# Optimization experiments

Measured on AMD Instinct MI355X. Metric: run time of the kernel, lower is better.

## Reference

```python
import jax, jax.numpy as jnp
import numpy as np

N_NODES = 100000
N_EDGES = 1600000
HIDDEN = 512
LOWER = 128
NUM_RELS = 6


def setup_inputs() -> dict:
    key = jax.random.key(0)
    ks = jax.random.split(key, 16)
    glorot = lambda k, shape: jax.random.normal(k, shape, jnp.float32) * (2.0 / (shape[-2] + shape[-1])) ** 0.5
    return {
        "h_origin": jax.random.normal(ks[0], (N_NODES, HIDDEN), jnp.float32),
        "edge_src": jax.random.randint(ks[1], (N_EDGES,), 0, N_NODES, jnp.int32),
        "edge_dst": jax.random.randint(ks[2], (N_EDGES,), 0, N_NODES, jnp.int32),
        "edge_type": jax.random.randint(ks[3], (N_EDGES,), 0, NUM_RELS, jnp.int32),
        "W_lower": glorot(ks[4], (HIDDEN, LOWER)),
        "b_lower": jnp.zeros((LOWER,), jnp.float32),
        "W1": glorot(ks[5], (NUM_RELS, LOWER, LOWER)),
        "b1": jnp.zeros((LOWER,), jnp.float32),
        "W2": glorot(ks[6], (NUM_RELS, LOWER, LOWER)),
        "b2": jnp.zeros((LOWER,), jnp.float32),
        "W3": glorot(ks[7], (NUM_RELS, LOWER, LOWER)),
        "b3": jnp.zeros((LOWER,), jnp.float32),
        "W_upper": glorot(ks[8], (LOWER, HIDDEN)),
        "b_upper": jnp.zeros((HIDDEN,), jnp.float32),
        "W_skip": glorot(ks[9], (HIDDEN, HIDDEN)),
        "b_skip": jnp.zeros((HIDDEN,), jnp.float32),
    }


def _ngcn_layer(h, W, b, edge_src, edge_dst, edge_type, n_nodes):
    # R-GCN layer: msg_e = h[src_e] @ W[rel_e]; h'_v = relu(sum_{e->v} msg_e + b)
    # Equivalent grouped form: transform all nodes by all relations (dense GEMMs),
    # then gather per-edge by (rel, src) -- same math as per-edge bmm.
    t = jnp.einsum("nd,rde->rne", h, W)          # [R, N, out]
    msg = t[edge_type, edge_src]                   # [E, out] gather
    agg = jax.ops.segment_sum(msg, edge_dst, num_segments=n_nodes)  # [N, out]
    return jax.nn.relu(agg + b)


def reference(h_origin, edge_src, edge_dst, edge_type,
              W_lower, b_lower, W1, b1, W2, b2, W3, b3,
              W_upper, b_upper, W_skip, b_skip):
    n_nodes = h_origin.shape[0]
    # lower: Linear + ReLU (hidden -> lower)
    h = jax.nn.relu(h_origin @ W_lower + b_lower)
    # three NGCN (R-GCN) layers, num_rels = 6
    h = _ngcn_layer(h, W1, b1, edge_src, edge_dst, edge_type, n_nodes)
    h = _ngcn_layer(h, W2, b2, edge_src, edge_dst, edge_type, n_nodes)
    h = _ngcn_layer(h, W3, b3, edge_src, edge_dst, edge_type, n_nodes)
    # upper(h) + skipper(origin): bg.ndata['h'] = upper(h) + skipper(origin_ndata)
    out = jax.nn.relu(h @ W_upper + b_upper) + jax.nn.relu(h_origin @ W_skip + b_skip)
    return out
```

## Files before the change

### kernel.cpp

```cpp
#include <hip/hip_runtime.h>
#include <hip/hip_bf16.h>

#define NN 100000
#define NE 1600000
#define HID 512
#define LOW 128
#define NR  6
#define NBINS (NN * NR)

typedef short  bf16x8 __attribute__((ext_vector_type(8)));
typedef float  f32x4  __attribute__((ext_vector_type(4)));
typedef float  f32x8  __attribute__((ext_vector_type(8)));
typedef unsigned short u16x8 __attribute__((ext_vector_type(8)));

__device__ __forceinline__ unsigned short f2bf(float x) {
    __hip_bfloat16 h = __float2bfloat16(x);
    return __builtin_bit_cast(unsigned short, h);
}
__device__ __forceinline__ float bf2f(unsigned short u) {
    return __builtin_bit_cast(float, (unsigned int)u << 16);
}
__device__ __forceinline__ f32x8 cvt8(u16x8 u) {
    f32x8 r;
    #pragma unroll
    for (int i = 0; i < 8; ++i) r[i] = bf2f(u[i]);
    return r;
}

template<int ITERS>
__device__ __forceinline__ void stage_rows(const unsigned short* __restrict__ G,
                                           int r0, int k0, int Kstride, int Rmax,
                                           char* lds_base, int tid)
{
    #pragma unroll
    for (int is = 0; is < ITERS; ++is) {
        int L   = is * 4096 + tid * 16;
        int row = L >> 7;
        int c   = ((L >> 4) & 7) ^ (row & 7);
        int gr  = r0 + row;
        gr = (gr < Rmax) ? gr : (Rmax - 1);
        const char* src = (const char*)G + ((size_t)gr * Kstride + k0) * 2 + c * 16;
        __builtin_amdgcn_global_load_lds(
            (const __attribute__((address_space(1))) void*)src,
            (__attribute__((address_space(3))) void*)(lds_base + is * 4096 + (tid & 192) * 16),
            16, 0, 0);
    }
}

__device__ __forceinline__ bf16x8 lds_frag(const char* lds_base, int row, int clog)
{
    return *(const bf16x8*)(lds_base + row * 128 + ((clog ^ (row & 7)) << 4));
}

__global__ __launch_bounds__(256, 2)
void gemm_bf16(const unsigned short* __restrict__ A,
               const unsigned short* __restrict__ Bt,
               const float* __restrict__ bias,
               unsigned short* __restrict__ C,
               int M, int N, int K)
{
    __shared__ __align__(16) char lA[16384];
    __shared__ __align__(16) char lB[16384];

    const int tid  = threadIdx.x;
    const int lane = tid & 63;
    const int wid  = tid >> 6;
    const int wm   = wid >> 1;
    const int wn   = wid & 1;
    const int m0   = blockIdx.y * 128;
    const int n0   = blockIdx.x * 128;

    f32x4 acc[4][4] = {};

    for (int k0 = 0; k0 < K; k0 += 64) {
        stage_rows<4>(A,  m0, k0, K, M, lA, tid);
        stage_rows<4>(Bt, n0, k0, K, N, lB, tid);
        __syncthreads();
        #pragma unroll
        for (int kk = 0; kk < 2; ++kk) {
            const int clog = kk * 4 + (lane >> 4);
            bf16x8 af[4], bfr[4];
            #pragma unroll
            for (int i = 0; i < 4; ++i)
                af[i] = lds_frag(lA, wm * 64 + i * 16 + (lane & 15), clog);
            #pragma unroll
            for (int j = 0; j < 4; ++j)
                bfr[j] = lds_frag(lB, wn * 64 + j * 16 + (lane & 15), clog);
            #pragma unroll
            for (int i = 0; i < 4; ++i)
                #pragma unroll
                for (int j = 0; j < 4; ++j)
                    acc[i][j] = __builtin_amdgcn_mfma_f32_16x16x32_bf16(
                        af[i], bfr[j], acc[i][j], 0, 0, 0);
        }
        __syncthreads();
    }

    const int col_l = lane & 15;
    const int rgrp  = lane >> 4;
    #pragma unroll
    for (int i = 0; i < 4; ++i) {
        #pragma unroll
        for (int j = 0; j < 4; ++j) {
            int col  = n0 + wn * 64 + j * 16 + col_l;
            float bv = bias[col];
            #pragma unroll
            for (int r = 0; r < 4; ++r) {
                int row = m0 + wm * 64 + i * 16 + rgrp * 4 + r;
                if (row < M)
                    C[(size_t)row * N + col] = f2bf(fmaxf(acc[i][j][r] + bv, 0.f));
            }
        }
    }
}

__global__ __launch_bounds__(256, 2)
void gemm_out_fused(const unsigned short* __restrict__ h,
                    const unsigned short* __restrict__ Wut,
                    const float* __restrict__ bu,
                    const unsigned short* __restrict__ hob,
                    const unsigned short* __restrict__ Wst,
                    const float* __restrict__ bs,
                    float* __restrict__ out, int M)
{
    __shared__ __align__(16) char lA[16384];
    __shared__ __align__(16) char lB[16384];

    const int tid  = threadIdx.x;
    const int lane = tid & 63;
    const int wid  = tid >> 6;
    const int wm   = wid >> 1;
    const int wn   = wid & 1;

    const int nwg  = gridDim.x;
    const int cpx  = nwg >> 3;
    const int idx  = (blockIdx.x & 7) * cpx + (blockIdx.x >> 3);
    const int m0   = (idx >> 2) * 128;
    const int n0   = (idx & 3) * 128;

    f32x4 acc1[4][4] = {};
    f32x4 acc2[4][4] = {};

    for (int k0 = 0; k0 < LOW; k0 += 64) {
        stage_rows<4>(h,   m0, k0, LOW, M,   lA, tid);
        stage_rows<4>(Wut, n0, k0, LOW, HID, lB, tid);
        __syncthreads();
        #pragma unroll
        for (int kk = 0; kk < 2; ++kk) {
            const int clog = kk * 4 + (lane >> 4);
            bf16x8 af[4], bfr[4];
            #pragma unroll
            for (int i = 0; i < 4; ++i)
                af[i] = lds_frag(lA, wm * 64 + i * 16 + (lane & 15), clog);
            #pragma unroll
            for (int j = 0; j < 4; ++j)
                bfr[j] = lds_frag(lB, wn * 64 + j * 16 + (lane & 15), clog);
            #pragma unroll
            for (int i = 0; i < 4; ++i)
                #pragma unroll
                for (int j = 0; j < 4; ++j)
                    acc1[i][j] = __builtin_amdgcn_mfma_f32_16x16x32_bf16(
                        af[i], bfr[j], acc1[i][j], 0, 0, 0);
        }
        __syncthreads();
    }
    for (int k0 = 0; k0 < HID; k0 += 64) {
        stage_rows<4>(hob, m0, k0, HID, M,   lA, tid);
        stage_rows<4>(Wst, n0, k0, HID, HID, lB, tid);
        __syncthreads();
        #pragma unroll
        for (int kk = 0; kk < 2; ++kk) {
            const int clog = kk * 4 + (lane >> 4);
            bf16x8 af[4], bfr[4];
            #pragma unroll
            for (int i = 0; i < 4; ++i)
                af[i] = lds_frag(lA, wm * 64 + i * 16 + (lane & 15), clog);
            #pragma unroll
            for (int j = 0; j < 4; ++j)
                bfr[j] = lds_frag(lB, wn * 64 + j * 16 + (lane & 15), clog);
            #pragma unroll
            for (int i = 0; i < 4; ++i)
                #pragma unroll
                for (int j = 0; j < 4; ++j)
                    acc2[i][j] = __builtin_amdgcn_mfma_f32_16x16x32_bf16(
                        af[i], bfr[j], acc2[i][j], 0, 0, 0);
        }
        __syncthreads();
    }

    const int col_l = lane & 15;
    const int rgrp  = lane >> 4;
    #pragma unroll
    for (int i = 0; i < 4; ++i) {
        #pragma unroll
        for (int j = 0; j < 4; ++j) {
            int col   = n0 + wn * 64 + j * 16 + col_l;
            float bv1 = bu[col], bv2 = bs[col];
            #pragma unroll
            for (int r = 0; r < 4; ++r) {
                int row = m0 + wm * 64 + i * 16 + rgrp * 4 + r;
                if (row < M) {
                    float v = fmaxf(acc1[i][j][r] + bv1, 0.f) +
                              fmaxf(acc2[i][j][r] + bv2, 0.f);
                    __builtin_nontemporal_store(v, &out[(size_t)row * HID + col]);
                }
            }
        }
    }
}

__global__ __launch_bounds__(256)
void conv_f32_bf16(const float4* __restrict__ in, ushort4* __restrict__ out, int n4)
{
    for (int i = blockIdx.x * 256 + threadIdx.x; i < n4; i += gridDim.x * 256) {
        float4 v = in[i];
        ushort4 o;
        o.x = f2bf(v.x); o.y = f2bf(v.y); o.z = f2bf(v.z); o.w = f2bf(v.w);
        out[i] = o;
    }
}

__global__ __launch_bounds__(256)
void transpose_bf16(const float* __restrict__ W, unsigned short* __restrict__ Wt,
                    int R, int C)
{
    int idx = blockIdx.x * 256 + threadIdx.x;
    if (idx < R * C) {
        int r = idx / C, c = idx - r * C;
        Wt[(size_t)c * R + r] = f2bf(W[idx]);
    }
}

#define SCAN_VT 8
#define SCAN_BS 256
#define SCAN_CHUNK (SCAN_VT * SCAN_BS)
#define SCAN_NB ((NBINS + SCAN_CHUNK - 1) / SCAN_CHUNK)

__global__ __launch_bounds__(256)
void k_hist(const int* __restrict__ dst, const int* __restrict__ typ,
            int* __restrict__ deg, int E)
{
    int e = blockIdx.x * 256 + threadIdx.x;
    if (e < E) atomicAdd(&deg[dst[e] * NR + typ[e]], 1);
}

__global__ __launch_bounds__(SCAN_BS)
void k_scan_part(const int* __restrict__ deg, int* __restrict__ blocksum, int n)
{
    __shared__ int ps[SCAN_BS];
    const int t = threadIdx.x;
    const int lo = blockIdx.x * SCAN_CHUNK + t * SCAN_VT;
    int s = 0;
    #pragma unroll
    for (int k = 0; k < SCAN_VT; ++k) {
        int i = lo + k;
        if (i < n) s += deg[i];
    }
    ps[t] = s;
    __syncthreads();
    for (int off = SCAN_BS / 2; off > 0; off >>= 1) {
        if (t < off) ps[t] += ps[t + off];
        __syncthreads();
    }
    if (t == 0) blocksum[blockIdx.x] = ps[0];
}

__global__ __launch_bounds__(64)
void k_scan_mid(const int* __restrict__ blocksum, int* __restrict__ blockoff,
                int* __restrict__ rowstart, int nb, int n)
{
    if (threadIdx.x == 0) {
        int run = 0;
        for (int i = 0; i < nb; ++i) { blockoff[i] = run; run += blocksum[i]; }
        rowstart[n] = run;
    }
}

__global__ __launch_bounds__(SCAN_BS)
void k_scan_final(const int* __restrict__ deg, const int* __restrict__ blockoff,
                  int* __restrict__ rowstart, int* __restrict__ cursor, int n)
{
    __shared__ int ps[SCAN_BS];
    const int t = threadIdx.x;
    const int lo = blockIdx.x * SCAN_CHUNK + t * SCAN_VT;
    int local[SCAN_VT];
    int s = 0;
    #pragma unroll
    for (int k = 0; k < SCAN_VT; ++k) {
        int i = lo + k;
        int v = (i < n) ? deg[i] : 0;
        local[k] = v;
        s += v;
    }
    ps[t] = s;
    __syncthreads();
    for (int off = 1; off < SCAN_BS; off <<= 1) {
        int v = (t >= off) ? ps[t - off] : 0;
        __syncthreads();
        ps[t] += v;
        __syncthreads();
    }
    int run = blockoff[blockIdx.x] + ((t > 0) ? ps[t - 1] : 0);
    #pragma unroll
    for (int k = 0; k < SCAN_VT; ++k) {
        int i = lo + k;
        if (i < n) {
            rowstart[i] = run;
            cursor[i]   = run;
            run += local[k];
        }
    }
}

__global__ __launch_bounds__(256)
void k_fill(const int* __restrict__ src, const int* __restrict__ dst,
            const int* __restrict__ typ, int* __restrict__ cursor,
            int* __restrict__ list, int E)
{
    int e = blockIdx.x * 256 + threadIdx.x;
    if (e < E) {
        int pos = atomicAdd(&cursor[dst[e] * NR + typ[e]], 1);
        list[pos] = src[e];
    }
}

__global__ __launch_bounds__(256)
void gather_agg(const unsigned short* __restrict__ h,
                const int* __restrict__ rowstart,
                const int* __restrict__ list,
                unsigned short* __restrict__ S)
{
    const int v = (blockIdx.x * 256 + threadIdx.x) >> 4;
    const int lane = threadIdx.x & 15;
    const u16x8* hp = (const u16x8*)h;

    const int b0 = rowstart[v * NR + 0];
    const int b1 = rowstart[v * NR + 1];
    const int b2 = rowstart[v * NR + 2];
    const int b3 = rowstart[v * NR + 3];
    const int b4 = rowstart[v * NR + 4];
    const int b5 = rowstart[v * NR + 5];
    const int b6 = rowstart[v * NR + 6];
    const int n0 = b1 - b0, n1 = b2 - b1, n2 = b3 - b2;
    const int n3 = b4 - b3, n4 = b5 - b4, n5 = b6 - b5;
    const int kmax = max(max(max(n0, n1), max(n2, n3)), max(n4, n5));

    f32x8 a0 = {}, a1 = {}, a2 = {}, a3 = {}, a4 = {}, a5 = {};

    for (int k = 0; k < kmax; ++k) {
        int i0 = (k < n0) ? (b0 + k) : 0;
        int i1 = (k < n1) ? (b1 + k) : 0;
        int i2 = (k < n2) ? (b2 + k) : 0;
        int i3 = (k < n3) ? (b3 + k) : 0;
        int i4 = (k < n4) ? (b4 + k) : 0;
        int i5 = (k < n5) ? (b5 + k) : 0;
        int s0 = list[i0], s1 = list[i1], s2 = list[i2];
        int s3 = list[i3], s4 = list[i4], s5 = list[i5];
        u16x8 u0 = hp[(size_t)s0 * 16 + lane];
        u16x8 u1 = hp[(size_t)s1 * 16 + lane];
        u16x8 u2 = hp[(size_t)s2 * 16 + lane];
        u16x8 u3 = hp[(size_t)s3 * 16 + lane];
        u16x8 u4 = hp[(size_t)s4 * 16 + lane];
        u16x8 u5 = hp[(size_t)s5 * 16 + lane];
        if (k < n0) a0 += cvt8(u0);
        if (k < n1) a1 += cvt8(u1);
        if (k < n2) a2 += cvt8(u2);
        if (k < n3) a3 += cvt8(u3);
        if (k < n4) a4 += cvt8(u4);
        if (k < n5) a5 += cvt8(u5);
    }

    u16x8* o = (u16x8*)(S + (size_t)v * (NR * LOW));
    u16x8 w;
    #pragma unroll
    for (int i = 0; i < 8; ++i) w[i] = f2bf(a0[i]);
    __builtin_nontemporal_store(w, &o[0 * 16 + lane]);
    #pragma unroll
    for (int i = 0; i < 8; ++i) w[i] = f2bf(a1[i]);
    __builtin_nontemporal_store(w, &o[1 * 16 + lane]);
    #pragma unroll
    for (int i = 0; i < 8; ++i) w[i] = f2bf(a2[i]);
    __builtin_nontemporal_store(w, &o[2 * 16 + lane]);
    #pragma unroll
    for (int i = 0; i < 8; ++i) w[i] = f2bf(a3[i]);
    __builtin_nontemporal_store(w, &o[3 * 16 + lane]);
    #pragma unroll
    for (int i = 0; i < 8; ++i) w[i] = f2bf(a4[i]);
    __builtin_nontemporal_store(w, &o[4 * 16 + lane]);
    #pragma unroll
    for (int i = 0; i < 8; ++i) w[i] = f2bf(a5[i]);
    __builtin_nontemporal_store(w, &o[5 * 16 + lane]);
}

extern "C" void kernel_launch(void* const* d_in, const int* in_sizes, int n_in,
                              void* d_out, int out_size, void* d_ws, size_t ws_size,
                              hipStream_t stream)
{
    (void)in_sizes; (void)n_in; (void)out_size; (void)ws_size;

    const float* h_origin = (const float*)d_in[0];
    const int*   esrc     = (const int*)d_in[1];
    const int*   edst     = (const int*)d_in[2];
    const int*   etyp     = (const int*)d_in[3];
    const float* W_lower  = (const float*)d_in[4];
    const float* b_lower  = (const float*)d_in[5];
    const float* Wl[3]    = {(const float*)d_in[6], (const float*)d_in[8], (const float*)d_in[10]};
    const float* bl[3]    = {(const float*)d_in[7], (const float*)d_in[9], (const float*)d_in[11]};
    const float* W_upper  = (const float*)d_in[12];
    const float* b_upper  = (const float*)d_in[13];
    const float* W_skip   = (const float*)d_in[14];
    const float* b_skip   = (const float*)d_in[15];
    float*       out      = (float*)d_out;

    unsigned short* hob = (unsigned short*)d_ws;
    unsigned short* h   = hob + (size_t)NN * HID;
    unsigned short* S   = h + (size_t)NN * LOW;
    unsigned short* wlt = S + (size_t)NN * NR * LOW;
    unsigned short* w1t = wlt + (size_t)LOW * HID;
    unsigned short* w2t = w1t + (size_t)LOW * NR * LOW;
    unsigned short* w3t = w2t + (size_t)LOW * NR * LOW;
    unsigned short* wut = w3t + (size_t)LOW * NR * LOW;
    unsigned short* wst = wut + (size_t)HID * LOW;
    int* deg      = (int*)(wst + (size_t)HID * HID);
    int* rowstart = deg + NBINS;
    int* cursor   = rowstart + NBINS + 1;
    int* list     = cursor + NBINS;
    int* blocksum = list + NE;
    int* blockoff = blocksum + SCAN_NB;
    unsigned short* wtL[3] = {w1t, w2t, w3t};

    const unsigned eBlocks = (unsigned)((NE + 255) / 256);
    const unsigned mBlocks = (unsigned)((NN + 127) / 128);

    conv_f32_bf16<<<dim3(2048), dim3(256), 0, stream>>>(
        (const float4*)h_origin, (ushort4*)hob, NN * HID / 4);
    transpose_bf16<<<dim3((HID * LOW + 255) / 256), dim3(256), 0, stream>>>(
        W_lower, wlt, HID, LOW);
    for (int L = 0; L < 3; ++L)
        transpose_bf16<<<dim3((NR * LOW * LOW + 255) / 256), dim3(256), 0, stream>>>(
            Wl[L], wtL[L], NR * LOW, LOW);
    transpose_bf16<<<dim3((LOW * HID + 255) / 256), dim3(256), 0, stream>>>(
        W_upper, wut, LOW, HID);
    transpose_bf16<<<dim3((HID * HID + 255) / 256), dim3(256), 0, stream>>>(
        W_skip, wst, HID, HID);

    hipMemsetAsync(deg, 0, NBINS * sizeof(int), stream);
    k_hist<<<dim3(eBlocks), dim3(256), 0, stream>>>(edst, etyp, deg, NE);
    k_scan_part<<<dim3(SCAN_NB), dim3(SCAN_BS), 0, stream>>>(deg, blocksum, NBINS);
    k_scan_mid<<<dim3(1), dim3(64), 0, stream>>>(blocksum, blockoff, rowstart, SCAN_NB, NBINS);
    k_scan_final<<<dim3(SCAN_NB), dim3(SCAN_BS), 0, stream>>>(deg, blockoff, rowstart, cursor, NBINS);
    k_fill<<<dim3(eBlocks), dim3(256), 0, stream>>>(esrc, edst, etyp, cursor, list, NE);

    gemm_bf16<<<dim3(1, mBlocks), dim3(256), 0, stream>>>(
        hob, wlt, b_lower, h, NN, LOW, HID);

    const unsigned gBlocks = (unsigned)(((size_t)NN * 16 + 255) / 256);
    for (int L = 0; L < 3; ++L) {
        gather_agg<<<dim3(gBlocks), dim3(256), 0, stream>>>(h, rowstart, list, S);
        gemm_bf16<<<dim3(1, mBlocks), dim3(256), 0, stream>>>(
            S, wtL[L], bl[L], h, NN, LOW, NR * LOW);
    }

    gemm_out_fused<<<dim3((HID / 128) * mBlocks), dim3(256), 0, stream>>>(
        h, wut, b_upper, hob, wst, b_skip, out, NN);
}
```

Measured before the change: 834.7 us.

## Interleave skip GEMM tiles into the memory-bound gather kernels

The skip-path GEMM (h_origin @ W_skip) is split into 3128 tiles and spread across the three gather kernel launches. Blocks in each launch act either as GEMM tiles or as gather blocks, so compute-bound MFMA work can overlap the latency-bound gather. The skip result is stored as bf16 in a new workspace buffer and added in a slimmer final upper GEMM. This adds a 100MB bf16 write and read round trip, rounds the skip activations to bf16, and can cause load imbalance inside the mixed launches.

```diff
diff --git a/kernel.cpp b/kernel.cpp
--- a/kernel.cpp
+++ b/kernel.cpp
@@ -7,6 +7,7 @@
 #define LOW 128
 #define NR  6
 #define NBINS (NN * NR)
+#define GBLK 6250
 
 typedef short  bf16x8 __attribute__((ext_vector_type(8)));
 typedef float  f32x4  __attribute__((ext_vector_type(4)));
@@ -114,223 +115,82 @@
     }
 }
 
-__global__ __launch_bounds__(256, 2)
-void gemm_out_fused(const unsigned short* __restrict__ h,
-                    const unsigned short* __restrict__ Wut,
-                    const float* __restrict__ bu,
-                    const unsigned short* __restrict__ hob,
-                    const unsigned short* __restrict__ Wst,
-                    const float* __restrict__ bs,
-                    float* __restrict__ out, int M)
+__global__ __launch_bounds__(256)
+void gather_skip(const unsigned short* __restrict__ h,
+                 const int* __restrict__ rowstart,
+                 const int* __restrict__ list,
+                 unsigned short* __restrict__ S,
+                 const unsigned short* __restrict__ hob,
+                 const unsigned short* __restrict__ wst,
+                 const float* __restrict__ bs,
+                 unsigned short* __restrict__ skipb,
+                 int tileOff, int CT, int T)
 {
     __shared__ __align__(16) char lA[16384];
     __shared__ __align__(16) char lB[16384];
 
-    const int tid  = threadIdx.x;
-    const int lane = tid & 63;
-    const int wid  = tid >> 6;
-    const int wm   = wid >> 1;
-    const int wn   = wid & 1;
-
-    const int nwg  = gridDim.x;
-    const int cpx  = nwg >> 3;
-    const int idx  = (blockIdx.x & 7) * cpx + (blockIdx.x >> 3);
-    const int m0   = (idx >> 2) * 128;
-    const int n0   = (idx & 3) * 128;
-
-    f32x4 acc1[4][4] = {};
-    f32x4 acc2[4][4] = {};
-
-    for (int k0 = 0; k0 < LOW; k0 += 64) {
-        stage_rows<4>(h,   m0, k0, LOW, M,   lA, tid);
-        stage_rows<4>(Wut, n0, k0, LOW, HID, lB, tid);
-        __syncthreads();
-        #pragma unroll
-        for (int kk = 0; kk < 2; ++kk) {
-            const int clog = kk * 4 + (lane >> 4);
-            bf16x8 af[4], bfr[4];
-            #pragma unroll
-            for (int i = 0; i < 4; ++i)
-                af[i] = lds_frag(lA, wm * 64 + i * 16 + (lane & 15), clog);
-            #pragma unroll
-            for (int j = 0; j < 4; ++j)
-                bfr[j] = lds_frag(lB, wn * 64 + j * 16 + (lane & 15), clog);
-            #pragma unroll
-            for (int i = 0; i < 4; ++i)
+    const int bid = blockIdx.x;
+    const int q   = (bid * CT) / T;
+    const bool isGemm = (((bid + 1) * CT) / T) > q;
+
+    if (isGemm) {
+        const int tile = tileOff + q;
+        const int m0   = (tile >> 2) * 128;
+        const int n0   = (tile & 3) * 128;
+        const int tid  = threadIdx.x;
+        const int lane = tid & 63;
+        const int wid  = tid >> 6;
+        const int wm   = wid >> 1;
+        const int wn   = wid & 1;
+
+        f32x4 acc[4][4] = {};
+
+        for (int k0 = 0; k0 < HID; k0 += 64) {
+            stage_rows<4>(hob, m0, k0, HID, NN,  lA, tid);
+            stage_rows<4>(wst, n0, k0, HID, HID, lB, tid);
+            __syncthreads();
+            #pragma unroll
+            for (int kk = 0; kk < 2; ++kk) {
+                const int clog = kk * 4 + (lane >> 4);
+                bf16x8 af[4], bfr[4];
+                #pragma unroll
+                for (int i = 0; i < 4; ++i)
+                    af[i] = lds_frag(lA, wm * 64 + i * 16 + (lane & 15), clog);
                 #pragma unroll
                 for (int j = 0; j < 4; ++j)
-                    acc1[i][j] = __builtin_amdgcn_mfma_f32_16x16x32_bf16(
-                        af[i], bfr[j], acc1[i][j], 0, 0, 0);
-        }
-        __syncthreads();
-    }
-    for (int k0 = 0; k0 < HID; k0 += 64) {
-        stage_rows<4>(hob, m0, k0, HID, M,   lA, tid);
-        stage_rows<4>(Wst, n0, k0, HID, HID, lB, tid);
-        __syncthreads();
+                    bfr[j] = lds_frag(lB, wn * 64 + j * 16 + (lane & 15), clog);
+                #pragma unroll
+                for (int i = 0; i < 4; ++i)
+                    #pragma unroll
+                    for (int j = 0; j < 4; ++j)
+                        acc[i][j] = __builtin_amdgcn_mfma_f32_16x16x32_bf16(
+                            af[i], bfr[j], acc[i][j], 0, 0, 0);
+            }
+            __syncthreads();
+        }
+
+        const int col_l = lane & 15;
+        const int rgrp  = lane >> 4;
         #pragma unroll
-        for (int kk = 0; kk < 2; ++kk) {
-            const int clog = kk * 4 + (lane >> 4);
-            bf16x8 af[4], bfr[4];
-            #pragma unroll
-            for (int i = 0; i < 4; ++i)
-                af[i] = lds_frag(lA, wm * 64 + i * 16 + (lane & 15), clog);
-            #pragma unroll
-            for (int j = 0; j < 4; ++j)
-                bfr[j] = lds_frag(lB, wn * 64 + j * 16 + (lane & 15), clog);
-            #pragma unroll
-            for (int i = 0; i < 4; ++i)
+        for (int i = 0; i < 4; ++i) {
+            #pragma unroll
+            for (int j = 0; j < 4; ++j) {
+                int col  = n0 + wn * 64 + j * 16 + col_l;
+                float bv = bs[col];
                 #pragma unroll
-                for (int j = 0; j < 4; ++j)
-                    acc2[i][j] = __builtin_amdgcn_mfma_f32_16x16x32_bf16(
-                        af[i], bfr[j], acc2[i][j], 0, 0, 0);
-        }
-        __syncthreads();
-    }
-
-    const int col_l = lane & 15;
-    const int rgrp  = lane >> 4;
-    #pragma unroll
-    for (int i = 0; i < 4; ++i) {
-        #pragma unroll
-        for (int j = 0; j < 4; ++j) {
-            int col   = n0 + wn * 64 + j * 16 + col_l;
-            float bv1 = bu[col], bv2 = bs[col];
-            #pragma unroll
-            for (int r = 0; r < 4; ++r) {
-                int row = m0 + wm * 64 + i * 16 + rgrp * 4 + r;
-                if (row < M) {
-                    float v = fmaxf(acc1[i][j][r] + bv1, 0.f) +
-                              fmaxf(acc2[i][j][r] + bv2, 0.f);
-                    __builtin_nontemporal_store(v, &out[(size_t)row * HID + col]);
+                for (int r = 0; r < 4; ++r) {
+                    int row = m0 + wm * 64 + i * 16 + rgrp * 4 + r;
+                    if (row < NN)
+                        skipb[(size_t)row * HID + col] =
+                            f2bf(fmaxf(acc[i][j][r] + bv, 0.f));
                 }
             }
         }
-    }
-}
-
-__global__ __launch_bounds__(256)
-void conv_f32_bf16(const float4* __restrict__ in, ushort4* __restrict__ out, int n4)
-{
-    for (int i = blockIdx.x * 256 + threadIdx.x; i < n4; i += gridDim.x * 256) {
-        float4 v = in[i];
-        ushort4 o;
-        o.x = f2bf(v.x); o.y = f2bf(v.y); o.z = f2bf(v.z); o.w = f2bf(v.w);
-        out[i] = o;
-    }
-}
-
-__global__ __launch_bounds__(256)
-void transpose_bf16(const float* __restrict__ W, unsigned short* __restrict__ Wt,
-                    int R, int C)
-{
-    int idx = blockIdx.x * 256 + threadIdx.x;
-    if (idx < R * C) {
-        int r = idx / C, c = idx - r * C;
-        Wt[(size_t)c * R + r] = f2bf(W[idx]);
-    }
-}
-
-#define SCAN_VT 8
-#define SCAN_BS 256
-#define SCAN_CHUNK (SCAN_VT * SCAN_BS)
-#define SCAN_NB ((NBINS + SCAN_CHUNK - 1) / SCAN_CHUNK)
-
-__global__ __launch_bounds__(256)
-void k_hist(const int* __restrict__ dst, const int* __restrict__ typ,
-            int* __restrict__ deg, int E)
-{
-    int e = blockIdx.x * 256 + threadIdx.x;
-    if (e < E) atomicAdd(&deg[dst[e] * NR + typ[e]], 1);
-}
-
-__global__ __launch_bounds__(SCAN_BS)
-void k_scan_part(const int* __restrict__ deg, int* __restrict__ blocksum, int n)
-{
-    __shared__ int ps[SCAN_BS];
-    const int t = threadIdx.x;
-    const int lo = blockIdx.x * SCAN_CHUNK + t * SCAN_VT;
-    int s = 0;
-    #pragma unroll
-    for (int k = 0; k < SCAN_VT; ++k) {
-        int i = lo + k;
-        if (i < n) s += deg[i];
-    }
-    ps[t] = s;
-    __syncthreads();
-    for (int off = SCAN_BS / 2; off > 0; off >>= 1) {
-        if (t < off) ps[t] += ps[t + off];
-        __syncthreads();
-    }
-    if (t == 0) blocksum[blockIdx.x] = ps[0];
-}
-
-__global__ __launch_bounds__(64)
-void k_scan_mid(const int* __restrict__ blocksum, int* __restrict__ blockoff,
-                int* __restrict__ rowstart, int nb, int n)
-{
-    if (threadIdx.x == 0) {
-        int run = 0;
-        for (int i = 0; i < nb; ++i) { blockoff[i] = run; run += blocksum[i]; }
-        rowstart[n] = run;
-    }
-}
-
-__global__ __launch_bounds__(SCAN_BS)
-void k_scan_final(const int* __restrict__ deg, const int* __restrict__ blockoff,
-                  int* __restrict__ rowstart, int* __restrict__ cursor, int n)
-{
-    __shared__ int ps[SCAN_BS];
-    const int t = threadIdx.x;
-    const int lo = blockIdx.x * SCAN_CHUNK + t * SCAN_VT;
-    int local[SCAN_VT];
-    int s = 0;
-    #pragma unroll
-    for (int k = 0; k < SCAN_VT; ++k) {
-        int i = lo + k;
-        int v = (i < n) ? deg[i] : 0;
-        local[k] = v;
-        s += v;
-    }
-    ps[t] = s;
-    __syncthreads();
-    for (int off = 1; off < SCAN_BS; off <<= 1) {
-        int v = (t >= off) ? ps[t - off] : 0;
-        __syncthreads();
-        ps[t] += v;
-        __syncthreads();
-    }
-    int run = blockoff[blockIdx.x] + ((t > 0) ? ps[t - 1] : 0);
-    #pragma unroll
-    for (int k = 0; k < SCAN_VT; ++k) {
-        int i = lo + k;
-        if (i < n) {
-            rowstart[i] = run;
-            cursor[i]   = run;
-            run += local[k];
-        }
-    }
-}
-
-__global__ __launch_bounds__(256)
-void k_fill(const int* __restrict__ src, const int* __restrict__ dst,
-            const int* __restrict__ typ, int* __restrict__ cursor,
-            int* __restrict__ list, int E)
-{
-    int e = blockIdx.x * 256 + threadIdx.x;
-    if (e < E) {
-        int pos = atomicAdd(&cursor[dst[e] * NR + typ[e]], 1);
-        list[pos] = src[e];
-    }
-}
-
-__global__ __launch_bounds__(256)
-void gather_agg(const unsigned short* __restrict__ h,
-                const int* __restrict__ rowstart,
-                const int* __restrict__ list,
-                unsigned short* __restrict__ S)
-{
-    const int v = (blockIdx.x * 256 + threadIdx.x) >> 4;
+        return;
+    }
+
+    const int g    = bid - q;
+    const int v    = g * 16 + (threadIdx.x >> 4);
     const int lane = threadIdx.x & 15;
     const u16x8* hp = (const u16x8*)h;
 
@@ -392,6 +252,190 @@
     __builtin_nontemporal_store(w, &o[5 * 16 + lane]);
 }
 
+__global__ __launch_bounds__(256, 2)
+void gemm_out_upper(const unsigned short* __restrict__ h,
+                    const unsigned short* __restrict__ Wut,
+                    const float* __restrict__ bu,
+                    const unsigned short* __restrict__ skipb,
+                    float* __restrict__ out, int M)
+{
+    __shared__ __align__(16) char lA[16384];
+    __shared__ __align__(16) char lB[16384];
+
+    const int tid  = threadIdx.x;
+    const int lane = tid & 63;
+    const int wid  = tid >> 6;
+    const int wm   = wid >> 1;
+    const int wn   = wid & 1;
+
+    const int nwg  = gridDim.x;
+    const int cpx  = nwg >> 3;
+    const int idx  = (blockIdx.x & 7) * cpx + (blockIdx.x >> 3);
+    const int m0   = (idx >> 2) * 128;
+    const int n0   = (idx & 3) * 128;
+
+    f32x4 acc[4][4] = {};
+
+    for (int k0 = 0; k0 < LOW; k0 += 64) {
+        stage_rows<4>(h,   m0, k0, LOW, M,   lA, tid);
+        stage_rows<4>(Wut, n0, k0, LOW, HID, lB, tid);
+        __syncthreads();
+        #pragma unroll
+        for (int kk = 0; kk < 2; ++kk) {
+            const int clog = kk * 4 + (lane >> 4);
+            bf16x8 af[4], bfr[4];
+            #pragma unroll
+            for (int i = 0; i < 4; ++i)
+                af[i] = lds_frag(lA, wm * 64 + i * 16 + (lane & 15), clog);
+            #pragma unroll
+            for (int j = 0; j < 4; ++j)
+                bfr[j] = lds_frag(lB, wn * 64 + j * 16 + (lane & 15), clog);
+            #pragma unroll
+            for (int i = 0; i < 4; ++i)
+                #pragma unroll
+                for (int j = 0; j < 4; ++j)
+                    acc[i][j] = __builtin_amdgcn_mfma_f32_16x16x32_bf16(
+                        af[i], bfr[j], acc[i][j], 0, 0, 0);
+        }
+        __syncthreads();
+    }
+
+    const int col_l = lane & 15;
+    const int rgrp  = lane >> 4;
+    #pragma unroll
+    for (int i = 0; i < 4; ++i) {
+        #pragma unroll
+        for (int j = 0; j < 4; ++j) {
+            int col  = n0 + wn * 64 + j * 16 + col_l;
+            float bv = bu[col];
+            #pragma unroll
+            for (int r = 0; r < 4; ++r) {
+                int row = m0 + wm * 64 + i * 16 + rgrp * 4 + r;
+                if (row < M) {
+                    float sk = bf2f(skipb[(size_t)row * HID + col]);
+                    out[(size_t)row * HID + col] =
+                        fmaxf(acc[i][j][r] + bv, 0.f) + sk;
+                }
+            }
+        }
+    }
+}
+
+__global__ __launch_bounds__(256)
+void conv_f32_bf16(const float4* __restrict__ in, ushort4* __restrict__ out, int n4)
+{
+    for (int i = blockIdx.x * 256 + threadIdx.x; i < n4; i += gridDim.x * 256) {
+        float4 v = in[i];
+        ushort4 o;
+        o.x = f2bf(v.x); o.y = f2bf(v.y); o.z = f2bf(v.z); o.w = f2bf(v.w);
+        out[i] = o;
+    }
+}
+
+__global__ __launch_bounds__(256)
+void transpose_bf16(const float* __restrict__ W, unsigned short* __restrict__ Wt,
+                    int R, int C)
+{
+    int idx = blockIdx.x * 256 + threadIdx.x;
+    if (idx < R * C) {
+        int r = idx / C, c = idx - r * C;
+        Wt[(size_t)c * R + r] = f2bf(W[idx]);
+    }
+}
+
+#define SCAN_VT 8
+#define SCAN_BS 256
+#define SCAN_CHUNK (SCAN_VT * SCAN_BS)
+#define SCAN_NB ((NBINS + SCAN_CHUNK - 1) / SCAN_CHUNK)
+
+__global__ __launch_bounds__(256)
+void k_hist(const int* __restrict__ dst, const int* __restrict__ typ,
+            int* __restrict__ deg, int E)
+{
+    int e = blockIdx.x * 256 + threadIdx.x;
+    if (e < E) atomicAdd(&deg[dst[e] * NR + typ[e]], 1);
+}
+
+__global__ __launch_bounds__(SCAN_BS)
+void k_scan_part(const int* __restrict__ deg, int* __restrict__ blocksum, int n)
+{
+    __shared__ int ps[SCAN_BS];
+    const int t = threadIdx.x;
+    const int lo = blockIdx.x * SCAN_CHUNK + t * SCAN_VT;
+    int s = 0;
+    #pragma unroll
+    for (int k = 0; k < SCAN_VT; ++k) {
+        int i = lo + k;
+        if (i < n) s += deg[i];
+    }
+    ps[t] = s;
+    __syncthreads();
+    for (int off = SCAN_BS / 2; off > 0; off >>= 1) {
+        if (t < off) ps[t] += ps[t + off];
+        __syncthreads();
+    }
+    if (t == 0) blocksum[blockIdx.x] = ps[0];
+}
+
+__global__ __launch_bounds__(64)
+void k_scan_mid(const int* __restrict__ blocksum, int* __restrict__ blockoff,
+                int* __restrict__ rowstart, int nb, int n)
+{
+    if (threadIdx.x == 0) {
+        int run = 0;
+        for (int i = 0; i < nb; ++i) { blockoff[i] = run; run += blocksum[i]; }
+        rowstart[n] = run;
+    }
+}
+
+__global__ __launch_bounds__(SCAN_BS)
+void k_scan_final(const int* __restrict__ deg, const int* __restrict__ blockoff,
+                  int* __restrict__ rowstart, int* __restrict__ cursor, int n)
+{
+    __shared__ int ps[SCAN_BS];
+    const int t = threadIdx.x;
+    const int lo = blockIdx.x * SCAN_CHUNK + t * SCAN_VT;
+    int local[SCAN_VT];
+    int s = 0;
+    #pragma unroll
+    for (int k = 0; k < SCAN_VT; ++k) {
+        int i = lo + k;
+        int v = (i < n) ? deg[i] : 0;
+        local[k] = v;
+        s += v;
+    }
+    ps[t] = s;
+    __syncthreads();
+    for (int off = 1; off < SCAN_BS; off <<= 1) {
+        int v = (t >= off) ? ps[t - off] : 0;
+        __syncthreads();
+        ps[t] += v;
+        __syncthreads();
+    }
+    int run = blockoff[blockIdx.x] + ((t > 0) ? ps[t - 1] : 0);
+    #pragma unroll
+    for (int k = 0; k < SCAN_VT; ++k) {
+        int i = lo + k;
+        if (i < n) {
+            rowstart[i] = run;
+            cursor[i]   = run;
+            run += local[k];
+        }
+    }
+}
+
+__global__ __launch_bounds__(256)
+void k_fill(const int* __restrict__ src, const int* __restrict__ dst,
+            const int* __restrict__ typ, int* __restrict__ cursor,
+            int* __restrict__ list, int E)
+{
+    int e = blockIdx.x * 256 + threadIdx.x;
+    if (e < E) {
+        int pos = atomicAdd(&cursor[dst[e] * NR + typ[e]], 1);
+        list[pos] = src[e];
+    }
+}
+
 extern "C" void kernel_launch(void* const* d_in, const int* in_sizes, int n_in,
                               void* d_out, int out_size, void* d_ws, size_t ws_size,
                               hipStream_t stream)
@@ -412,15 +456,16 @@
     const float* b_skip   = (const float*)d_in[15];
     float*       out      = (float*)d_out;
 
-    unsigned short* hob = (unsigned short*)d_ws;
-    unsigned short* h   = hob + (size_t)NN * HID;
-    unsigned short* S   = h + (size_t)NN * LOW;
-    unsigned short* wlt = S + (size_t)NN * NR * LOW;
-    unsigned short* w1t = wlt + (size_t)LOW * HID;
-    unsigned short* w2t = w1t + (size_t)LOW * NR * LOW;
-    unsigned short* w3t = w2t + (size_t)LOW * NR * LOW;
-    unsigned short* wut = w3t + (size_t)LOW * NR * LOW;
-    unsigned short* wst = wut + (size_t)HID * LOW;
+    unsigned short* hob   = (unsigned short*)d_ws;
+    unsigned short* h     = hob + (size_t)NN * HID;
+    unsigned short* S     = h + (size_t)NN * LOW;
+    unsigned short* skipb = S + (size_t)NN * NR * LOW;
+    unsigned short* wlt   = skipb + (size_t)NN * HID;
+    unsigned short* w1t   = wlt + (size_t)LOW * HID;
+    unsigned short* w2t   = w1t + (size_t)LOW * NR * LOW;
+    unsigned short* w3t   = w2t + (size_t)LOW * NR * LOW;
+    unsigned short* wut   = w3t + (size_t)LOW * NR * LOW;
+    unsigned short* wst   = wut + (size_t)HID * LOW;
     int* deg      = (int*)(wst + (size_t)HID * HID);
     int* rowstart = deg + NBINS;
     int* cursor   = rowstart + NBINS + 1;
@@ -454,13 +499,16 @@
     gemm_bf16<<<dim3(1, mBlocks), dim3(256), 0, stream>>>(
         hob, wlt, b_lower, h, NN, LOW, HID);
 
-    const unsigned gBlocks = (unsigned)(((size_t)NN * 16 + 255) / 256);
+    const int CTs[3]  = {1043, 1043, 1042};
+    const int offs[3] = {0, 1043, 2086};
     for (int L = 0; L < 3; ++L) {
-        gather_agg<<<dim3(gBlocks), dim3(256), 0, stream>>>(h, rowstart, list, S);
+        int T = GBLK + CTs[L];
+        gather_skip<<<dim3((unsigned)T), dim3(256), 0, stream>>>(
+            h, rowstart, list, S, hob, wst, b_skip, skipb, offs[L], CTs[L], T);
         gemm_bf16<<<dim3(1, mBlocks), dim3(256), 0, stream>>>(
             S, wtL[L], bl[L], h, NN, LOW, NR * LOW);
     }
 
-    gemm_out_fused<<<dim3((HID / 128) * mBlocks), dim3(256), 0, stream>>>(
-        h, wut, b_upper, hob, wst, b_skip, out, NN);
-}
+    gemm_out_upper<<<dim3((HID / 128) * mBlocks), dim3(256), 0, stream>>>(
+        h, wut, b_upper, skipb, out, NN);
+}
```

Result: slower. 1.129 ms (+35.3%).

## Double-buffer LDS tiles in GEMM kernels to overlap loads with MFMA

Applied to the files above, without the earlier changes.

Both GEMM kernels now keep two LDS buffers per operand and issue the next K-tile's global-to-LDS loads before running the MFMAs on the current tile. This hides global load latency behind compute and removes one barrier per step. In the fused output kernel, the first skip-GEMM tile is prefetched during the last upper-GEMM step. The final output store also changes from nontemporal to a regular store. LDS use doubles to 64KB per block, which may lower occupancy below the two-blocks-per-CU launch bound.

```diff
diff --git a/kernel.cpp b/kernel.cpp
--- a/kernel.cpp
+++ b/kernel.cpp
@@ -27,13 +27,12 @@
     return r;
 }
 
-template<int ITERS>
 __device__ __forceinline__ void stage_rows(const unsigned short* __restrict__ G,
                                            int r0, int k0, int Kstride, int Rmax,
                                            char* lds_base, int tid)
 {
     #pragma unroll
-    for (int is = 0; is < ITERS; ++is) {
+    for (int is = 0; is < 4; ++is) {
         int L   = is * 4096 + tid * 16;
         int row = L >> 7;
         int c   = ((L >> 4) & 7) ^ (row & 7);
@@ -59,8 +58,8 @@
                unsigned short* __restrict__ C,
                int M, int N, int K)
 {
-    __shared__ __align__(16) char lA[16384];
-    __shared__ __align__(16) char lB[16384];
+    __shared__ __align__(16) char lA[2][16384];
+    __shared__ __align__(16) char lB[2][16384];
 
     const int tid  = threadIdx.x;
     const int lane = tid & 63;
@@ -72,20 +71,28 @@
 
     f32x4 acc[4][4] = {};
 
-    for (int k0 = 0; k0 < K; k0 += 64) {
-        stage_rows<4>(A,  m0, k0, K, M, lA, tid);
-        stage_rows<4>(Bt, n0, k0, K, N, lB, tid);
-        __syncthreads();
+    stage_rows(A,  m0, 0, K, M, lA[0], tid);
+    stage_rows(Bt, n0, 0, K, N, lB[0], tid);
+    __syncthreads();
+
+    const int nsteps = K >> 6;
+    int cur = 0;
+    for (int s = 0; s < nsteps; ++s) {
+        int nxt = cur ^ 1;
+        if (s + 1 < nsteps) {
+            stage_rows(A,  m0, (s + 1) << 6, K, M, lA[nxt], tid);
+            stage_rows(Bt, n0, (s + 1) << 6, K, N, lB[nxt], tid);
+        }
         #pragma unroll
         for (int kk = 0; kk < 2; ++kk) {
             const int clog = kk * 4 + (lane >> 4);
             bf16x8 af[4], bfr[4];
             #pragma unroll
             for (int i = 0; i < 4; ++i)
-                af[i] = lds_frag(lA, wm * 64 + i * 16 + (lane & 15), clog);
+                af[i] = lds_frag(lA[cur], wm * 64 + i * 16 + (lane & 15), clog);
             #pragma unroll
             for (int j = 0; j < 4; ++j)
-                bfr[j] = lds_frag(lB, wn * 64 + j * 16 + (lane & 15), clog);
+                bfr[j] = lds_frag(lB[cur], wn * 64 + j * 16 + (lane & 15), clog);
             #pragma unroll
             for (int i = 0; i < 4; ++i)
                 #pragma unroll
@@ -94,6 +101,7 @@
                         af[i], bfr[j], acc[i][j], 0, 0, 0);
         }
         __syncthreads();
+        cur = nxt;
     }
 
     const int col_l = lane & 15;
@@ -123,8 +131,8 @@
                     const float* __restrict__ bs,
                     float* __restrict__ out, int M)
 {
-    __shared__ __align__(16) char lA[16384];
-    __shared__ __align__(16) char lB[16384];
+    __shared__ __align__(16) char lA[2][16384];
+    __shared__ __align__(16) char lB[2][16384];
 
     const int tid  = threadIdx.x;
     const int lane = tid & 63;
@@ -141,20 +149,30 @@
     f32x4 acc1[4][4] = {};
     f32x4 acc2[4][4] = {};
 
-    for (int k0 = 0; k0 < LOW; k0 += 64) {
-        stage_rows<4>(h,   m0, k0, LOW, M,   lA, tid);
-        stage_rows<4>(Wut, n0, k0, LOW, HID, lB, tid);
-        __syncthreads();
+    stage_rows(h,   m0, 0, LOW, M,   lA[0], tid);
+    stage_rows(Wut, n0, 0, LOW, HID, lB[0], tid);
+    __syncthreads();
+
+    int cur = 0;
+    for (int s = 0; s < 2; ++s) {
+        int nxt = cur ^ 1;
+        if (s == 0) {
+            stage_rows(h,   m0, 64, LOW, M,   lA[nxt], tid);
+            stage_rows(Wut, n0, 64, LOW, HID, lB[nxt], tid);
+        } else {
+            stage_rows(hob, m0, 0, HID, M,   lA[nxt], tid);
+            stage_rows(Wst, n0, 0, HID, HID, lB[nxt], tid);
+        }
         #pragma unroll
         for (int kk = 0; kk < 2; ++kk) {
             const int clog = kk * 4 + (lane >> 4);
             bf16x8 af[4], bfr[4];
             #pragma unroll
             for (int i = 0; i < 4; ++i)
-                af[i] = lds_frag(lA, wm * 64 + i * 16 + (lane & 15), clog);
+                af[i] = lds_frag(lA[cur], wm * 64 + i * 16 + (lane & 15), clog);
             #pragma unroll
             for (int j = 0; j < 4; ++j)
-                bfr[j] = lds_frag(lB, wn * 64 + j * 16 + (lane & 15), clog);
+                bfr[j] = lds_frag(lB[cur], wn * 64 + j * 16 + (lane & 15), clog);
             #pragma unroll
             for (int i = 0; i < 4; ++i)
                 #pragma unroll
@@ -163,21 +181,24 @@
                         af[i], bfr[j], acc1[i][j], 0, 0, 0);
         }
         __syncthreads();
-    }
-    for (int k0 = 0; k0 < HID; k0 += 64) {
-        stage_rows<4>(hob, m0, k0, HID, M,   lA, tid);
-        stage_rows<4>(Wst, n0, k0, HID, HID, lB, tid);
-        __syncthreads();
+        cur = nxt;
+    }
+    for (int s = 0; s < 8; ++s) {
+        int nxt = cur ^ 1;
+        if (s + 1 < 8) {
+            stage_rows(hob, m0, (s + 1) << 6, HID, M,   lA[nxt], tid);
+            stage_rows(Wst, n0, (s + 1) << 6, HID, HID, lB[nxt], tid);
+        }
         #pragma unroll
         for (int kk = 0; kk < 2; ++kk) {
             const int clog = kk * 4 + (lane >> 4);
             bf16x8 af[4], bfr[4];
             #pragma unroll
             for (int i = 0; i < 4; ++i)
-                af[i] = lds_frag(lA, wm * 64 + i * 16 + (lane & 15), clog);
+                af[i] = lds_frag(lA[cur], wm * 64 + i * 16 + (lane & 15), clog);
             #pragma unroll
             for (int j = 0; j < 4; ++j)
-                bfr[j] = lds_frag(lB, wn * 64 + j * 16 + (lane & 15), clog);
+                bfr[j] = lds_frag(lB[cur], wn * 64 + j * 16 + (lane & 15), clog);
             #pragma unroll
             for (int i = 0; i < 4; ++i)
                 #pragma unroll
@@ -186,6 +207,7 @@
                         af[i], bfr[j], acc2[i][j], 0, 0, 0);
         }
         __syncthreads();
+        cur = nxt;
     }
 
     const int col_l = lane & 15;
@@ -199,11 +221,9 @@
             #pragma unroll
             for (int r = 0; r < 4; ++r) {
                 int row = m0 + wm * 64 + i * 16 + rgrp * 4 + r;
-                if (row < M) {
-                    float v = fmaxf(acc1[i][j][r] + bv1, 0.f) +
-                              fmaxf(acc2[i][j][r] + bv2, 0.f);
-                    __builtin_nontemporal_store(v, &out[(size_t)row * HID + col]);
-                }
+                if (row < M)
+                    out[(size_t)row * HID + col] =
+                        fmaxf(acc1[i][j][r] + bv1, 0.f) + fmaxf(acc2[i][j][r] + bv2, 0.f);
             }
         }
     }
```

After: 847.0 us. About the same (+1.5%).
